# Optimization experiments

Measured on AMD Instinct MI355X. Metric: run time of the kernel, lower is better.

## Reference

```python
import jax, jax.numpy as jnp
import numpy as np

B, S, H, NH = 2, 2048, 2048, 16
HD = H // NH  # head_dim = 128


def setup_inputs() -> dict:
    key = jax.random.key(0)
    ks = jax.random.split(key, 6)
    scale = 1.0 / np.sqrt(H)
    hidden_state = jax.random.normal(ks[0], (B, S, H), dtype=jnp.float32)
    # upper-triangular (strictly above diagonal) = 1 -> masked positions
    causal_mask = jnp.triu(jnp.ones((S, S), dtype=jnp.float32), k=1)[None, None]
    Wq = jax.random.normal(ks[1], (H, H), dtype=jnp.float32) * scale
    Wk = jax.random.normal(ks[2], (H, H), dtype=jnp.float32) * scale
    Wv = jax.random.normal(ks[3], (H, H), dtype=jnp.float32) * scale
    Wo = jax.random.normal(ks[4], (H, H), dtype=jnp.float32) * scale
    zeros = jnp.zeros((H,), dtype=jnp.float32)
    return {"hidden_state": hidden_state, "causal_mask": causal_mask,
            "Wq": Wq, "bq": zeros, "Wk": Wk, "bk": zeros,
            "Wv": Wv, "bv": zeros, "Wo": Wo, "bo": zeros}


def reference(hidden_state, causal_mask, Wq, bq, Wk, bk, Wv, bv, Wo, bo):
    b, s, h = hidden_state.shape
    q = (hidden_state @ Wq.T + bq).reshape(b, s, NH, HD).transpose(0, 2, 1, 3)  # [B,NH,S,HD]
    k = (hidden_state @ Wk.T + bk).reshape(b, s, NH, HD).transpose(0, 2, 1, 3)
    v = (hidden_state @ Wv.T + bv).reshape(b, s, NH, HD).transpose(0, 2, 1, 3)
    scores = jnp.einsum('bhqd,bhkd->bhqk', q, k) / jnp.sqrt(jnp.float32(HD))
    scores = scores + causal_mask * (-1e9)
    probs = jax.nn.softmax(scores, axis=-1)
    out = jnp.einsum('bhqk,bhkd->bhqd', probs, v)
    out = out.transpose(0, 2, 1, 3).reshape(b, s, h)
    return out @ Wo.T + bo
```

## Files before the change

### kernel.cpp

```cpp
#include <hip/hip_runtime.h>
#include <hip/hip_bf16.h>
#include <stdint.h>

#define B_   2
#define S_   2048
#define H_   2048
#define NH_  16
#define HD_  128
#define MTOT (B_*S_)

typedef __attribute__((ext_vector_type(8))) short bf16x8;
typedef __attribute__((ext_vector_type(4))) float f32x4;

__device__ __forceinline__ void gload_lds16(const void* g, void* l) {
    __builtin_amdgcn_global_load_lds(
        (const __attribute__((address_space(1))) void*)g,
        (__attribute__((address_space(3))) void*)l, 16, 0, 0);
}

__device__ __forceinline__ unsigned short f2bfu(float x) {
    __hip_bfloat16 h = __float2bfloat16(x);
    return *reinterpret_cast<unsigned short*>(&h);
}
__device__ __forceinline__ int packbf(float a, float b) {
    return (int)f2bfu(a) | ((int)f2bfu(b) << 16);
}

__global__ void castk(const float* __restrict__ in, __hip_bfloat16* __restrict__ out, int n4) {
    int i = blockIdx.x * 256 + threadIdx.x;
    if (i < n4) {
        float4 v = *(const float4*)(in + (size_t)i * 4);
        out[(size_t)i*4 + 0] = __float2bfloat16(v.x);
        out[(size_t)i*4 + 1] = __float2bfloat16(v.y);
        out[(size_t)i*4 + 2] = __float2bfloat16(v.z);
        out[(size_t)i*4 + 3] = __float2bfloat16(v.w);
    }
}

__global__ void castw4(const float* __restrict__ w0, const float* __restrict__ w1,
                       const float* __restrict__ w2, const float* __restrict__ w3,
                       __hip_bfloat16* o0, __hip_bfloat16* o1,
                       __hip_bfloat16* o2, __hip_bfloat16* o3, int n4) {
    const float* in; __hip_bfloat16* out;
    switch (blockIdx.y) {
        case 0:  in = w0; out = o0; break;
        case 1:  in = w1; out = o1; break;
        case 2:  in = w2; out = o2; break;
        default: in = w3; out = o3; break;
    }
    int i = blockIdx.x * 256 + threadIdx.x;
    if (i < n4) {
        float4 v = *(const float4*)(in + (size_t)i * 4);
        out[(size_t)i*4 + 0] = __float2bfloat16(v.x);
        out[(size_t)i*4 + 1] = __float2bfloat16(v.y);
        out[(size_t)i*4 + 2] = __float2bfloat16(v.z);
        out[(size_t)i*4 + 3] = __float2bfloat16(v.w);
    }
}

template<int SMEMB, int BF16OUT>
__device__ __forceinline__ void gemm_body(const __hip_bfloat16* __restrict__ Ablk,
                                          const __hip_bfloat16* __restrict__ Wblk,
                                          const float* __restrict__ bias,
                                          void* __restrict__ Cout,
                                          int N, int K, int br, int bc, bool vt)
{
    __shared__ __align__(16) char smem[SMEMB];
    __hip_bfloat16* As = (__hip_bfloat16*)smem;
    __hip_bfloat16* Bs = (__hip_bfloat16*)(smem + 8192);

    const int tid  = threadIdx.x;
    const int wave = tid >> 6, lane = tid & 63;
    const int quad = lane >> 4, l16 = lane & 15;
    const int wr = wave >> 1, wc = wave & 1;

    f32x4 acc[4][4] = {};

    for (int k0 = 0; k0 < K; k0 += 32) {
#pragma unroll
        for (int t = 0; t < 2; ++t) {
            int c = t * 256 + wave * 64 + lane;
            int row = c >> 2, cc = c & 3;
            int base = (t * 256 + wave * 64) * 16;
            gload_lds16(Ablk + (size_t)row * K + k0 + cc * 8, (char*)As + base);
            gload_lds16(Wblk + (size_t)row * K + k0 + cc * 8, (char*)Bs + base);
        }
        __syncthreads();

        bf16x8 af[4], bf[4];
#pragma unroll
        for (int i = 0; i < 4; ++i)
            af[i] = *(const bf16x8*)&As[(wr * 64 + i * 16 + l16) * 32 + quad * 8];
#pragma unroll
        for (int j = 0; j < 4; ++j)
            bf[j] = *(const bf16x8*)&Bs[(wc * 64 + j * 16 + l16) * 32 + quad * 8];

#pragma unroll
        for (int i = 0; i < 4; ++i)
#pragma unroll
            for (int j = 0; j < 4; ++j)
                acc[i][j] = __builtin_amdgcn_mfma_f32_16x16x32_bf16(af[i], bf[j], acc[i][j], 0, 0, 0);
        __syncthreads();
    }

    if (BF16OUT && vt) {
        __hip_bfloat16* Ls = (__hip_bfloat16*)smem;
#pragma unroll
        for (int j = 0; j < 4; ++j) {
            int d = wc * 64 + j * 16 + l16;
            float bv = bias[bc * 128 + d];
#pragma unroll
            for (int i = 0; i < 4; ++i) {
                int t0 = wr * 64 + i * 16 + quad * 4;
#pragma unroll
                for (int r = 0; r < 4; ++r)
                    Ls[d * 136 + t0 + r] = __float2bfloat16(acc[i][j][r] + bv);
            }
        }
        __syncthreads();
        const int bq = br >> 4;
        const int s0 = (br & 15) * 128;
        __hip_bfloat16* VT = (__hip_bfloat16*)Cout;
        const size_t rowbase = (size_t)(bq * 16 + bc) * 128;
#pragma unroll
        for (int rep = 0; rep < 8; ++rep) {
            int L = rep * 256 + tid;
            int d = L >> 4, tch = L & 15;
            bf16x8 v = *(const bf16x8*)&Ls[d * 136 + tch * 8];
            *(bf16x8*)(VT + (rowbase + d) * (size_t)S_ + s0 + tch * 8) = v;
        }
        return;
    }

#pragma unroll
    for (int i = 0; i < 4; ++i) {
        int row = br * 128 + wr * 64 + i * 16 + quad * 4;
#pragma unroll
        for (int j = 0; j < 4; ++j) {
            int col = bc * 128 + wc * 64 + j * 16 + l16;
            float bv = bias[col];
#pragma unroll
            for (int r = 0; r < 4; ++r) {
                float v = acc[i][j][r] + bv;
                if (BF16OUT)
                    ((__hip_bfloat16*)Cout)[(size_t)(row + r) * N + col] = __float2bfloat16(v);
                else
                    ((float*)Cout)[(size_t)(row + r) * N + col] = v;
            }
        }
    }
}

__global__ __launch_bounds__(256)
void gemm_qkv(const __hip_bfloat16* __restrict__ X,
              const __hip_bfloat16* __restrict__ Wq, const __hip_bfloat16* __restrict__ Wk,
              const __hip_bfloat16* __restrict__ Wv,
              const float* __restrict__ bq, const float* __restrict__ bk,
              const float* __restrict__ bv,
              __hip_bfloat16* Qo, __hip_bfloat16* Ko, __hip_bfloat16* VTo)
{
    const int sel = blockIdx.x >> 4;
    const int bc  = blockIdx.x & 15;
    const int br  = blockIdx.y;
    const __hip_bfloat16* W = (sel == 0) ? Wq : (sel == 1) ? Wk : Wv;
    const float* bias       = (sel == 0) ? bq : (sel == 1) ? bk : bv;
    void* out               = (sel == 0) ? (void*)Qo : (sel == 1) ? (void*)Ko : (void*)VTo;
    gemm_body<34816, 1>(X + (size_t)(br * 128) * H_, W + (size_t)(bc * 128) * H_,
                        bias, out, H_, H_, br, bc, sel == 2);
}

__global__ __launch_bounds__(256)
void gemm_out(const __hip_bfloat16* __restrict__ A, const __hip_bfloat16* __restrict__ W,
              const float* __restrict__ bias, float* __restrict__ C)
{
    gemm_body<16384, 0>(A + (size_t)(blockIdx.y * 128) * H_, W + (size_t)(blockIdx.x * 128) * H_,
                        bias, C, H_, H_, blockIdx.y, blockIdx.x, false);
}

__global__ __launch_bounds__(256)
void attn_kernel(const __hip_bfloat16* __restrict__ Q,
                 const __hip_bfloat16* __restrict__ K,
                 const __hip_bfloat16* __restrict__ VT,
                 __hip_bfloat16* __restrict__ O)
{
    __shared__ __align__(16) char KsB[2][16384];
    __shared__ __align__(16) char VtB[2][16384];

    const int tid  = threadIdx.x;
    const int wave = tid >> 6, lane = tid & 63;
    const int quad = lane >> 4, l16 = lane & 15;

    const int lid  = blockIdx.x;
    const int xcd  = lid & 7;
    const int slot = lid >> 3;
    const int bh   = ((slot >> 4) << 3) | xcd;
    const int pr   = slot & 15;
    const int b    = bh >> 4, h = bh & 15;

    const size_t headoff = (size_t)b * S_ * H_ + (size_t)h * HD_;
    const __hip_bfloat16* Qp = Q + headoff;
    const __hip_bfloat16* Kp = K + headoff;
    const __hip_bfloat16* Vtp = VT + (size_t)(b * 16 + h) * 128 * S_;

    const float scale = 0.08838834764831843f;
    const int A0 = (((quad & 1) * 2) * 16 + l16) * 4;
    const int A1 = A0 + 64;
    const bool hiq = (quad >= 2);

    for (int which = 0; which < 2; ++which) {
        const int qb = which ? pr : 31 - pr;
        const int qrow_local = wave * 16;
        const int qrow = qb * 64 + qrow_local;

        bf16x8 qf[4];
#pragma unroll
        for (int kd = 0; kd < 4; ++kd)
            qf[kd] = *(const bf16x8*)(Qp + (size_t)(qrow + l16) * H_ + kd * 32 + quad * 8);

        f32x4 oacc[8] = {};
        float mi = -1e30f, li = 0.0f;
        int bb = 0;

#pragma unroll
        for (int t = 0; t < 4; ++t) {
            int c = wave * 256 + t * 64 + lane;
            int krow = c >> 4, kpos = c & 15;
            gload_lds16(Kp + (size_t)krow * H_ + (kpos ^ (krow & 7)) * 8,
                        &KsB[0][(wave * 256 + t * 64) * 16]);
            int vrow = c >> 3, vpos = c & 7;
            gload_lds16(Vtp + (size_t)vrow * S_ + (vpos ^ (vrow & 7)) * 8,
                        &VtB[0][(wave * 256 + t * 64) * 16]);
        }
        __syncthreads();

        for (int kb = 0; kb <= qb; ++kb) {
            const int nb = bb ^ 1;
            if (kb < qb) {
                const __hip_bfloat16* Kn = Kp + (size_t)(kb + 1) * 64 * H_;
                const int vcol = (kb + 1) * 64;
#pragma unroll
                for (int t = 0; t < 4; ++t) {
                    int c = wave * 256 + t * 64 + lane;
                    int krow = c >> 4, kpos = c & 15;
                    gload_lds16(Kn + (size_t)krow * H_ + (kpos ^ (krow & 7)) * 8,
                                &KsB[nb][(wave * 256 + t * 64) * 16]);
                    int vrow = c >> 3, vpos = c & 7;
                    gload_lds16(Vtp + (size_t)vrow * S_ + vcol + (vpos ^ (vrow & 7)) * 8,
                                &VtB[nb][(wave * 256 + t * 64) * 16]);
                }
            }

            f32x4 sacc[4] = {};
#pragma unroll
            for (int cb = 0; cb < 4; ++cb) {
#pragma unroll
                for (int kd = 0; kd < 4; ++kd) {
                    int row = cb * 16 + l16;
                    int pos = (4 * kd + quad) ^ (l16 & 7);
                    bf16x8 kf = *(const bf16x8*)&KsB[bb][row * 256 + pos * 16];
                    sacc[cb] = __builtin_amdgcn_mfma_f32_16x16x32_bf16(kf, qf[kd], sacc[cb], 0, 0, 0);
                }
            }

            const bool diag = (kb == qb);
            float p[4][4];
            float tm = -1e30f;
#pragma unroll
            for (int cb = 0; cb < 4; ++cb)
#pragma unroll
                for (int r = 0; r < 4; ++r) {
                    float s = sacc[cb][r] * scale;
                    if (diag) {
                        int keyl = cb * 16 + quad * 4 + r;
                        if (keyl > qrow_local + l16) s = -1e30f;
                    }
                    p[cb][r] = s;
                    tm = fmaxf(tm, s);
                }
            tm = fmaxf(tm, __shfl_xor(tm, 16));
            tm = fmaxf(tm, __shfl_xor(tm, 32));
            float mnew = fmaxf(mi, tm);
            float sum = 0.0f;
#pragma unroll
            for (int cb = 0; cb < 4; ++cb)
#pragma unroll
                for (int r = 0; r < 4; ++r) {
                    float e = __expf(p[cb][r] - mnew);
                    p[cb][r] = e;
                    sum += e;
                }
            sum += __shfl_xor(sum, 16);
            sum += __shfl_xor(sum, 32);
            float alpha = __expf(mi - mnew);
            li = li * alpha + sum;
            mi = mnew;

            float ar[4];
#pragma unroll
            for (int r = 0; r < 4; ++r)
                ar[r] = __shfl(alpha, quad * 4 + r);
#pragma unroll
            for (int db = 0; db < 8; ++db)
#pragma unroll
                for (int r = 0; r < 4; ++r)
                    oacc[db][r] *= ar[r];

            int Pp[4][2];
#pragma unroll
            for (int cb = 0; cb < 4; ++cb) {
                Pp[cb][0] = packbf(p[cb][0], p[cb][1]);
                Pp[cb][1] = packbf(p[cb][2], p[cb][3]);
            }
            bf16x8 pf[2];
#pragma unroll
            for (int ks = 0; ks < 2; ++ks) {
                int c0 = 2 * ks, c1 = 2 * ks + 1;
                int d0 = __builtin_amdgcn_ds_bpermute(A0, Pp[c0][0]);
                int e0 = __builtin_amdgcn_ds_bpermute(A0, Pp[c1][0]);
                int d1 = __builtin_amdgcn_ds_bpermute(A0, Pp[c0][1]);
                int e1 = __builtin_amdgcn_ds_bpermute(A0, Pp[c1][1]);
                int d2 = __builtin_amdgcn_ds_bpermute(A1, Pp[c0][0]);
                int e2 = __builtin_amdgcn_ds_bpermute(A1, Pp[c1][0]);
                int d3 = __builtin_amdgcn_ds_bpermute(A1, Pp[c0][1]);
                int e3 = __builtin_amdgcn_ds_bpermute(A1, Pp[c1][1]);
                union { int i[4]; bf16x8 v; } u;
                u.i[0] = hiq ? e0 : d0;
                u.i[1] = hiq ? e1 : d1;
                u.i[2] = hiq ? e2 : d2;
                u.i[3] = hiq ? e3 : d3;
                pf[ks] = u.v;
            }

#pragma unroll
            for (int ks = 0; ks < 2; ++ks) {
#pragma unroll
                for (int db = 0; db < 8; ++db) {
                    int vrow = db * 16 + l16;
                    int vpos = (ks * 4 + quad) ^ (l16 & 7);
                    bf16x8 vf = *(const bf16x8*)&VtB[bb][vrow * 128 + vpos * 16];
                    oacc[db] = __builtin_amdgcn_mfma_f32_16x16x32_bf16(pf[ks], vf, oacc[db], 0, 0, 0);
                }
            }

            __syncthreads();
            bb = nb;
        }

        float lr[4];
#pragma unroll
        for (int r = 0; r < 4; ++r)
            lr[r] = __shfl(li, quad * 4 + r);
#pragma unroll
        for (int db = 0; db < 8; ++db)
#pragma unroll
            for (int r = 0; r < 4; ++r) {
                float v = oacc[db][r] / lr[r];
                size_t row = (size_t)b * S_ + qrow + quad * 4 + r;
                O[row * H_ + h * HD_ + db * 16 + l16] = __float2bfloat16(v);
            }
    }
}

extern "C" void kernel_launch(void* const* d_in, const int* in_sizes, int n_in,
                              void* d_out, int out_size, void* d_ws, size_t ws_size,
                              hipStream_t stream)
{
    const float* hs = (const float*)d_in[0];
    const float* Wq = (const float*)d_in[2];
    const float* bq = (const float*)d_in[3];
    const float* Wk = (const float*)d_in[4];
    const float* bk = (const float*)d_in[5];
    const float* Wv = (const float*)d_in[6];
    const float* bv = (const float*)d_in[7];
    const float* Wo = (const float*)d_in[8];
    const float* bo = (const float*)d_in[9];

    const size_t szX = (size_t)MTOT * H_;
    const size_t szW = (size_t)H_ * H_;

    __hip_bfloat16* Xbf = (__hip_bfloat16*)d_ws;
    __hip_bfloat16* Wqb = Xbf + szX;
    __hip_bfloat16* Wkb = Wqb + szW;
    __hip_bfloat16* Wvb = Wkb + szW;
    __hip_bfloat16* Wob = Wvb + szW;
    __hip_bfloat16* Qb  = Wob + szW;
    __hip_bfloat16* Kb  = Qb + szX;
    __hip_bfloat16* VTb = Kb + szX;

    castk<<<(int)((szX/4 + 255)/256), 256, 0, stream>>>(hs, Xbf, (int)(szX/4));
    dim3 wgrid((unsigned)((szW/4 + 255)/256), 4);
    castw4<<<wgrid, 256, 0, stream>>>(Wq, Wk, Wv, Wo, Wqb, Wkb, Wvb, Wob, (int)(szW/4));

    gemm_qkv<<<dim3(48, 32), 256, 0, stream>>>(Xbf, Wqb, Wkb, Wvb, bq, bk, bv, Qb, Kb, VTb);

    attn_kernel<<<dim3(512), 256, 0, stream>>>(Qb, Kb, VTb, Xbf);

    gemm_out<<<dim3(16, 32), 256, 0, stream>>>(Xbf, Wob, bo, (float*)d_out);
}
```

Before: 422.1 us.

## Use single-buffered K/V staging with split loads and one q-block per workgroup

The attention kernel drops the paired-q-block loop, so each workgroup handles one 64-row query block, and the grid doubles from 512 to 1024 blocks. K and V tiles move from double buffers to single buffers. The next K tile is loaded right after QK^T finishes and the next V tile after PV, with barriers in between. This halves LDS use per block to raise occupancy and gives more parallelism, but costs some load overlap and loses the balanced causal pairing, since blocks now vary in work (scheduled longest first).

```diff
diff --git a/kernel.cpp b/kernel.cpp
--- a/kernel.cpp
+++ b/kernel.cpp
@@ -183,23 +183,23 @@
                  const __hip_bfloat16* __restrict__ VT,
                  __hip_bfloat16* __restrict__ O)
 {
-    __shared__ __align__(16) char KsB[2][16384];
-    __shared__ __align__(16) char VtB[2][16384];
+    __shared__ __align__(16) char Ks[16384];
+    __shared__ __align__(16) char Vt[16384];
 
     const int tid  = threadIdx.x;
     const int wave = tid >> 6, lane = tid & 63;
     const int quad = lane >> 4, l16 = lane & 15;
 
-    const int lid  = blockIdx.x;
-    const int xcd  = lid & 7;
-    const int slot = lid >> 3;
-    const int bh   = ((slot >> 4) << 3) | xcd;
-    const int pr   = slot & 15;
-    const int b    = bh >> 4, h = bh & 15;
+    const int lid = blockIdx.x;
+    const int xcd = lid & 7;
+    const int q   = lid >> 3;
+    const int bh  = ((q >> 5) << 3) | xcd;
+    const int qb  = 31 - (q & 31);
+    const int b   = bh >> 4, h = bh & 15;
 
     const size_t headoff = (size_t)b * S_ * H_ + (size_t)h * HD_;
-    const __hip_bfloat16* Qp = Q + headoff;
-    const __hip_bfloat16* Kp = K + headoff;
+    const __hip_bfloat16* Qp  = Q + headoff;
+    const __hip_bfloat16* Kp  = K + headoff;
     const __hip_bfloat16* Vtp = VT + (size_t)(b * 16 + h) * 128 * S_;
 
     const float scale = 0.08838834764831843f;
@@ -207,158 +207,163 @@
     const int A1 = A0 + 64;
     const bool hiq = (quad >= 2);
 
-    for (int which = 0; which < 2; ++which) {
-        const int qb = which ? pr : 31 - pr;
-        const int qrow_local = wave * 16;
-        const int qrow = qb * 64 + qrow_local;
-
-        bf16x8 qf[4];
-#pragma unroll
-        for (int kd = 0; kd < 4; ++kd)
-            qf[kd] = *(const bf16x8*)(Qp + (size_t)(qrow + l16) * H_ + kd * 32 + quad * 8);
-
-        f32x4 oacc[8] = {};
-        float mi = -1e30f, li = 0.0f;
-        int bb = 0;
-
-#pragma unroll
-        for (int t = 0; t < 4; ++t) {
-            int c = wave * 256 + t * 64 + lane;
-            int krow = c >> 4, kpos = c & 15;
-            gload_lds16(Kp + (size_t)krow * H_ + (kpos ^ (krow & 7)) * 8,
-                        &KsB[0][(wave * 256 + t * 64) * 16]);
-            int vrow = c >> 3, vpos = c & 7;
-            gload_lds16(Vtp + (size_t)vrow * S_ + (vpos ^ (vrow & 7)) * 8,
-                        &VtB[0][(wave * 256 + t * 64) * 16]);
-        }
+    const int qrow_local = wave * 16;
+    const int qrow = qb * 64 + qrow_local;
+
+    bf16x8 qf[4];
+#pragma unroll
+    for (int kd = 0; kd < 4; ++kd)
+        qf[kd] = *(const bf16x8*)(Qp + (size_t)(qrow + l16) * H_ + kd * 32 + quad * 8);
+
+    f32x4 oacc[8] = {};
+    float mi = -1e30f, li = 0.0f;
+
+#pragma unroll
+    for (int t = 0; t < 4; ++t) {
+        int c = wave * 256 + t * 64 + lane;
+        int krow = c >> 4, kpos = c & 15;
+        gload_lds16(Kp + (size_t)krow * H_ + (kpos ^ (krow & 7)) * 8,
+                    &Ks[(wave * 256 + t * 64) * 16]);
+        int vrow = c >> 3, vpos = c & 7;
+        gload_lds16(Vtp + (size_t)vrow * S_ + (vpos ^ (vrow & 7)) * 8,
+                    &Vt[(wave * 256 + t * 64) * 16]);
+    }
+    __syncthreads();
+
+    for (int kb = 0; kb <= qb; ++kb) {
+        const bool more = (kb < qb);
+
+        f32x4 sacc[4] = {};
+#pragma unroll
+        for (int cb = 0; cb < 4; ++cb) {
+#pragma unroll
+            for (int kd = 0; kd < 4; ++kd) {
+                int row = cb * 16 + l16;
+                int pos = (4 * kd + quad) ^ (l16 & 7);
+                bf16x8 kf = *(const bf16x8*)&Ks[row * 256 + pos * 16];
+                sacc[cb] = __builtin_amdgcn_mfma_f32_16x16x32_bf16(kf, qf[kd], sacc[cb], 0, 0, 0);
+            }
+        }
+
         __syncthreads();
 
-        for (int kb = 0; kb <= qb; ++kb) {
-            const int nb = bb ^ 1;
-            if (kb < qb) {
-                const __hip_bfloat16* Kn = Kp + (size_t)(kb + 1) * 64 * H_;
-                const int vcol = (kb + 1) * 64;
-#pragma unroll
-                for (int t = 0; t < 4; ++t) {
-                    int c = wave * 256 + t * 64 + lane;
-                    int krow = c >> 4, kpos = c & 15;
-                    gload_lds16(Kn + (size_t)krow * H_ + (kpos ^ (krow & 7)) * 8,
-                                &KsB[nb][(wave * 256 + t * 64) * 16]);
-                    int vrow = c >> 3, vpos = c & 7;
-                    gload_lds16(Vtp + (size_t)vrow * S_ + vcol + (vpos ^ (vrow & 7)) * 8,
-                                &VtB[nb][(wave * 256 + t * 64) * 16]);
+        if (more) {
+            const __hip_bfloat16* Kn = Kp + (size_t)(kb + 1) * 64 * H_;
+#pragma unroll
+            for (int t = 0; t < 4; ++t) {
+                int c = wave * 256 + t * 64 + lane;
+                int krow = c >> 4, kpos = c & 15;
+                gload_lds16(Kn + (size_t)krow * H_ + (kpos ^ (krow & 7)) * 8,
+                            &Ks[(wave * 256 + t * 64) * 16]);
+            }
+        }
+
+        const bool diag = (kb == qb);
+        float p[4][4];
+        float tm = -1e30f;
+#pragma unroll
+        for (int cb = 0; cb < 4; ++cb)
+#pragma unroll
+            for (int r = 0; r < 4; ++r) {
+                float s = sacc[cb][r] * scale;
+                if (diag) {
+                    int keyl = cb * 16 + quad * 4 + r;
+                    if (keyl > qrow_local + l16) s = -1e30f;
                 }
-            }
-
-            f32x4 sacc[4] = {};
-#pragma unroll
-            for (int cb = 0; cb < 4; ++cb) {
-#pragma unroll
-                for (int kd = 0; kd < 4; ++kd) {
-                    int row = cb * 16 + l16;
-                    int pos = (4 * kd + quad) ^ (l16 & 7);
-                    bf16x8 kf = *(const bf16x8*)&KsB[bb][row * 256 + pos * 16];
-                    sacc[cb] = __builtin_amdgcn_mfma_f32_16x16x32_bf16(kf, qf[kd], sacc[cb], 0, 0, 0);
-                }
-            }
-
-            const bool diag = (kb == qb);
-            float p[4][4];
-            float tm = -1e30f;
-#pragma unroll
-            for (int cb = 0; cb < 4; ++cb)
-#pragma unroll
-                for (int r = 0; r < 4; ++r) {
-                    float s = sacc[cb][r] * scale;
-                    if (diag) {
-                        int keyl = cb * 16 + quad * 4 + r;
-                        if (keyl > qrow_local + l16) s = -1e30f;
-                    }
-                    p[cb][r] = s;
-                    tm = fmaxf(tm, s);
-                }
-            tm = fmaxf(tm, __shfl_xor(tm, 16));
-            tm = fmaxf(tm, __shfl_xor(tm, 32));
-            float mnew = fmaxf(mi, tm);
-            float sum = 0.0f;
-#pragma unroll
-            for (int cb = 0; cb < 4; ++cb)
-#pragma unroll
-                for (int r = 0; r < 4; ++r) {
-                    float e = __expf(p[cb][r] - mnew);
-                    p[cb][r] = e;
-                    sum += e;
-                }
-            sum += __shfl_xor(sum, 16);
-            sum += __shfl_xor(sum, 32);
-            float alpha = __expf(mi - mnew);
-            li = li * alpha + sum;
-            mi = mnew;
-
-            float ar[4];
+                p[cb][r] = s;
+                tm = fmaxf(tm, s);
+            }
+        tm = fmaxf(tm, __shfl_xor(tm, 16));
+        tm = fmaxf(tm, __shfl_xor(tm, 32));
+        float mnew = fmaxf(mi, tm);
+        float sum = 0.0f;
+#pragma unroll
+        for (int cb = 0; cb < 4; ++cb)
+#pragma unroll
+            for (int r = 0; r < 4; ++r) {
+                float e = __expf(p[cb][r] - mnew);
+                p[cb][r] = e;
+                sum += e;
+            }
+        sum += __shfl_xor(sum, 16);
+        sum += __shfl_xor(sum, 32);
+        float alpha = __expf(mi - mnew);
+        li = li * alpha + sum;
+        mi = mnew;
+
+        float ar[4];
+#pragma unroll
+        for (int r = 0; r < 4; ++r)
+            ar[r] = __shfl(alpha, quad * 4 + r);
+#pragma unroll
+        for (int db = 0; db < 8; ++db)
 #pragma unroll
             for (int r = 0; r < 4; ++r)
-                ar[r] = __shfl(alpha, quad * 4 + r);
-#pragma unroll
-            for (int db = 0; db < 8; ++db)
-#pragma unroll
-                for (int r = 0; r < 4; ++r)
-                    oacc[db][r] *= ar[r];
-
-            int Pp[4][2];
-#pragma unroll
-            for (int cb = 0; cb < 4; ++cb) {
-                Pp[cb][0] = packbf(p[cb][0], p[cb][1]);
-                Pp[cb][1] = packbf(p[cb][2], p[cb][3]);
-            }
-            bf16x8 pf[2];
-#pragma unroll
-            for (int ks = 0; ks < 2; ++ks) {
-                int c0 = 2 * ks, c1 = 2 * ks + 1;
-                int d0 = __builtin_amdgcn_ds_bpermute(A0, Pp[c0][0]);
-                int e0 = __builtin_amdgcn_ds_bpermute(A0, Pp[c1][0]);
-                int d1 = __builtin_amdgcn_ds_bpermute(A0, Pp[c0][1]);
-                int e1 = __builtin_amdgcn_ds_bpermute(A0, Pp[c1][1]);
-                int d2 = __builtin_amdgcn_ds_bpermute(A1, Pp[c0][0]);
-                int e2 = __builtin_amdgcn_ds_bpermute(A1, Pp[c1][0]);
-                int d3 = __builtin_amdgcn_ds_bpermute(A1, Pp[c0][1]);
-                int e3 = __builtin_amdgcn_ds_bpermute(A1, Pp[c1][1]);
-                union { int i[4]; bf16x8 v; } u;
-                u.i[0] = hiq ? e0 : d0;
-                u.i[1] = hiq ? e1 : d1;
-                u.i[2] = hiq ? e2 : d2;
-                u.i[3] = hiq ? e3 : d3;
-                pf[ks] = u.v;
-            }
-
-#pragma unroll
-            for (int ks = 0; ks < 2; ++ks) {
-#pragma unroll
-                for (int db = 0; db < 8; ++db) {
-                    int vrow = db * 16 + l16;
-                    int vpos = (ks * 4 + quad) ^ (l16 & 7);
-                    bf16x8 vf = *(const bf16x8*)&VtB[bb][vrow * 128 + vpos * 16];
-                    oacc[db] = __builtin_amdgcn_mfma_f32_16x16x32_bf16(pf[ks], vf, oacc[db], 0, 0, 0);
-                }
-            }
-
-            __syncthreads();
-            bb = nb;
-        }
-
-        float lr[4];
-#pragma unroll
-        for (int r = 0; r < 4; ++r)
-            lr[r] = __shfl(li, quad * 4 + r);
-#pragma unroll
-        for (int db = 0; db < 8; ++db)
-#pragma unroll
-            for (int r = 0; r < 4; ++r) {
-                float v = oacc[db][r] / lr[r];
-                size_t row = (size_t)b * S_ + qrow + quad * 4 + r;
-                O[row * H_ + h * HD_ + db * 16 + l16] = __float2bfloat16(v);
-            }
-    }
+                oacc[db][r] *= ar[r];
+
+        int Pp[4][2];
+#pragma unroll
+        for (int cb = 0; cb < 4; ++cb) {
+            Pp[cb][0] = packbf(p[cb][0], p[cb][1]);
+            Pp[cb][1] = packbf(p[cb][2], p[cb][3]);
+        }
+        bf16x8 pf[2];
+#pragma unroll
+        for (int ks = 0; ks < 2; ++ks) {
+            int c0 = 2 * ks, c1 = 2 * ks + 1;
+            int d0 = __builtin_amdgcn_ds_bpermute(A0, Pp[c0][0]);
+            int e0 = __builtin_amdgcn_ds_bpermute(A0, Pp[c1][0]);
+            int d1 = __builtin_amdgcn_ds_bpermute(A0, Pp[c0][1]);
+            int e1 = __builtin_amdgcn_ds_bpermute(A0, Pp[c1][1]);
+            int d2 = __builtin_amdgcn_ds_bpermute(A1, Pp[c0][0]);
+            int e2 = __builtin_amdgcn_ds_bpermute(A1, Pp[c1][0]);
+            int d3 = __builtin_amdgcn_ds_bpermute(A1, Pp[c0][1]);
+            int e3 = __builtin_amdgcn_ds_bpermute(A1, Pp[c1][1]);
+            union { int i[4]; bf16x8 v; } u;
+            u.i[0] = hiq ? e0 : d0;
+            u.i[1] = hiq ? e1 : d1;
+            u.i[2] = hiq ? e2 : d2;
+            u.i[3] = hiq ? e3 : d3;
+            pf[ks] = u.v;
+        }
+
+#pragma unroll
+        for (int ks = 0; ks < 2; ++ks) {
+#pragma unroll
+            for (int db = 0; db < 8; ++db) {
+                int vrow = db * 16 + l16;
+                int vpos = (ks * 4 + quad) ^ (l16 & 7);
+                bf16x8 vf = *(const bf16x8*)&Vt[vrow * 128 + vpos * 16];
+                oacc[db] = __builtin_amdgcn_mfma_f32_16x16x32_bf16(pf[ks], vf, oacc[db], 0, 0, 0);
+            }
+        }
+
+        __syncthreads();
+
+        if (more) {
+            const int vcol = (kb + 1) * 64;
+#pragma unroll
+            for (int t = 0; t < 4; ++t) {
+                int c = wave * 256 + t * 64 + lane;
+                int vrow = c >> 3, vpos = c & 7;
+                gload_lds16(Vtp + (size_t)vrow * S_ + vcol + (vpos ^ (vrow & 7)) * 8,
+                            &Vt[(wave * 256 + t * 64) * 16]);
+            }
+        }
+    }
+
+    float lr[4];
+#pragma unroll
+    for (int r = 0; r < 4; ++r)
+        lr[r] = __shfl(li, quad * 4 + r);
+#pragma unroll
+    for (int db = 0; db < 8; ++db)
+#pragma unroll
+        for (int r = 0; r < 4; ++r) {
+            float v = oacc[db][r] / lr[r];
+            size_t row = (size_t)b * S_ + qrow + quad * 4 + r;
+            O[row * H_ + h * HD_ + db * 16 + l16] = __float2bfloat16(v);
+        }
 }
 
 extern "C" void kernel_launch(void* const* d_in, const int* in_sizes, int n_in,
@@ -393,7 +398,7 @@
 
     gemm_qkv<<<dim3(48, 32), 256, 0, stream>>>(Xbf, Wqb, Wkb, Wvb, bq, bk, bv, Qb, Kb, VTb);
 
-    attn_kernel<<<dim3(512), 256, 0, stream>>>(Qb, Kb, VTb, Xbf);
+    attn_kernel<<<dim3(1024), 256, 0, stream>>>(Qb, Kb, VTb, Xbf);
 
     gemm_out<<<dim3(16, 32), 256, 0, stream>>>(Xbf, Wob, bo, (float*)d_out);
 }
```

After: 413.6 us. 1.02x faster.
